# Kernel tuning notes

Measured on AMD Instinct MI355X. Metric: run time of the kernel, lower is better.

Reference implementation:

```python
import jax, jax.numpy as jnp
import numpy as np

# Model/config dims
N_NODE = 500000   # num_node (item vocab)
D      = 100      # opt.hiddenSize
B      = 512      # batch
S      = 50       # session seq len
NS     = 12       # opt.n_sample neighbors per node
HOP    = 1        # opt.n_iter
STEP   = 1        # opt.step (star-graph propagation steps)
LAST   = 3        # opt.last_len
NADJ   = 12       # adjacent items per last item
SCALE  = 1.0 / np.sqrt(D)


def setup_inputs() -> dict:
    key = jax.random.key(0)
    ks = jax.random.split(key, 16)
    stdv = 1.0 / np.sqrt(D)
    u = lambda k, sh: jax.random.uniform(k, sh, jnp.float32, -stdv, stdv)
    return {
        # forward args
        "inputs":     jax.random.randint(ks[0], (B, S), 0, N_NODE),
        "adj":        jax.random.uniform(ks[1], (B, S, S), jnp.float32),
        "item":       jax.random.randint(ks[2], (B, S), 0, N_NODE),
        "last_items": jax.random.randint(ks[3], (B, LAST), 0, N_NODE),
        "adj_items":  jax.random.randint(ks[4], (B, LAST * NADJ), 0, N_NODE),
        # learned params / buffers
        "embedding": u(ks[5], (N_NODE, D)),
        "s":         u(ks[6], (2, 1)),
        "W_star_a":  u(ks[7], (D, D)),
        "W_star_q":  u(ks[8], (D, D)),
        "W_star_k":  u(ks[9], (D, D)),
        "W_g":       u(ks[10], (2 * D, D)),
        "W_l":       u(ks[11], (D, D)),
        "adj_all":   jax.random.randint(ks[12], (N_NODE, NS), 0, N_NODE),
        "num_w":     jax.random.uniform(ks[13], (N_NODE, NS), jnp.float32),
    }


def _l2norm(x):
    # F.normalize(p=2, dim=-1)
    return x / jnp.maximum(jnp.linalg.norm(x, axis=-1, keepdims=True), 1e-12)


def reference(inputs, adj, item, last_items, adj_items,
              embedding, s, W_star_a, W_star_q, W_star_k, W_g, W_l,
              adj_all, num_w):
    # ----- embedding lookup + padding mask -----
    h = embedding[inputs]                                  # [B,S,D]
    mask = (inputs != 0).astype(h.dtype)                   # [B,S]

    # ----- StarAggregator (local branch): star node + gated propagation -----
    denom = jnp.maximum(mask.sum(-1, keepdims=True), 1.0)
    star = (h * mask[..., None]).sum(1) / denom            # [B,D] masked mean
    hl = h
    for _ in range(STEP):
        h_n = jnp.einsum('bst,btd->bsd', adj, hl @ W_star_a)          # neighbor agg
        gate = jax.nn.sigmoid(
            jnp.einsum('bsd,bd->bs', hl @ W_star_q, star @ W_star_k) * SCALE)
        hl = (1.0 - gate)[..., None] * h_n + gate[..., None] * star[:, None, :]
        beta = jnp.einsum('bsd,bd->bs', hl, star) * SCALE
        beta = jax.nn.softmax(jnp.where(mask > 0, beta, -1e9), axis=1)
        star = jnp.einsum('bs,bsd->bd', beta, hl)
    h_local = hl                                           # [B,S,D]

    # ----- GlobalAggregator (hop=1 neighbor-sampling branch) -----
    flat = inputs.reshape(-1)
    neigh_idx = adj_all[flat].reshape(B, S, NS)            # gathered neighbor ids
    neigh_w = num_w[flat].reshape(B, S, NS)                # co-occurrence weights
    neigh = embedding[neigh_idx]                           # [B,S,NS,D]
    alpha = jax.nn.softmax(neigh_w, axis=-1)
    agg = jnp.einsum('bsn,bsnd->bsd', alpha, neigh)        # weighted neighbor sum
    h_global = jax.nn.relu(jnp.concatenate([h, agg], -1) @ W_g)  # [B,S,D]

    # ----- normalize + (eval-mode dropout = identity) + learned 2-way combine -----
    h_local = _l2norm(h_local)
    h_global = _l2norm(h_global)
    output = jnp.einsum('bsdk,ko->bsdo',
                        jnp.stack([h_local, h_global], axis=-1), s)[..., 0]  # [B,S,D]

    # ----- LastAggregator (last-items attention branch) -----
    item_h = embedding[last_items]                         # [B,L,D]
    adj_h = embedding[adj_items].reshape(B, LAST, -1, D)   # [B,L,NADJ,D]
    q = item_h @ W_l
    att = jax.nn.softmax(jnp.einsum('bld,blnd->bln', q, adj_h) * SCALE, axis=-1)
    aggl = jnp.einsum('bln,blnd->bld', att, adj_h)
    last_hidden = (item_h + aggl).mean(axis=1)             # [B,D]

    return output, last_hidden
```

## Files before the change

### kernel.cpp

```cpp
#include <hip/hip_runtime.h>
#include <hip/hip_fp16.h>

#define B_    512
#define S_    50
#define D_    100
#define NS_   12
#define LAST_ 3
#define NADJ_ 12
#define SCALE_ 0.1f

typedef __attribute__((ext_vector_type(4))) float f4;

__device__ __forceinline__ f4 ntload4(const float* p) {
    return __builtin_nontemporal_load((const f4*)p);
}

#define GEMM_STEP(ACC, BUF, K, W0, W1, W2, W3)                                      \
    _Pragma("unroll")                                                                \
    for (int i = 0; i < 5; ++i) {                                                    \
        float4 x = *(const float4*)&BUF[sb + i][K];                                  \
        ACC[i][0] = fmaf(x.x,W0.x, fmaf(x.y,W1.x, fmaf(x.z,W2.x, fmaf(x.w,W3.x, ACC[i][0])))); \
        ACC[i][1] = fmaf(x.x,W0.y, fmaf(x.y,W1.y, fmaf(x.z,W2.y, fmaf(x.w,W3.y, ACC[i][1])))); \
        ACC[i][2] = fmaf(x.x,W0.z, fmaf(x.y,W1.z, fmaf(x.z,W2.z, fmaf(x.w,W3.z, ACC[i][2])))); \
        ACC[i][3] = fmaf(x.x,W0.w, fmaf(x.y,W1.w, fmaf(x.z,W2.w, fmaf(x.w,W3.w, ACC[i][3])))); \
    }

#define AGG_ISSUE(I)                                                                 \
    {   int base = (sb + (I)) * NS_;                                                 \
        _Pragma("unroll")                                                            \
        for (int n = 0; n < NS_; ++n)                                                \
            q[n] = ntload4(emb + nid[base + n] * D_ + d4);                           \
    }
#define AGG_CONSUME(I)                                                               \
    {   int base = (sb + (I)) * NS_;                                                 \
        float mx = -1e30f;                                                           \
        _Pragma("unroll")                                                            \
        for (int n = 0; n < NS_; ++n) mx = fmaxf(mx, alf[base + n]);                 \
        float agw[NS_]; float sm = 0.f;                                              \
        _Pragma("unroll")                                                            \
        for (int n = 0; n < NS_; ++n) { agw[n] = __expf(alf[base + n] - mx); sm += agw[n]; } \
        float inv = 1.f / sm;                                                        \
        _Pragma("unroll")                                                            \
        for (int n = 0; n < NS_; ++n) {                                              \
            float w = agw[n] * inv;                                                  \
            agg[I][0] = fmaf(w, q[n].x, agg[I][0]);                                  \
            agg[I][1] = fmaf(w, q[n].y, agg[I][1]);                                  \
            agg[I][2] = fmaf(w, q[n].z, agg[I][2]);                                  \
            agg[I][3] = fmaf(w, q[n].w, agg[I][3]);                                  \
        }                                                                            \
    }

__global__ __launch_bounds__(256, 3) void fused_all(
    const int* __restrict__ inputs,
    const float* __restrict__ adj,
    const float* __restrict__ emb,
    const int* __restrict__ adj_all,
    const float* __restrict__ num_w,
    const float* __restrict__ sW,
    const float* __restrict__ Wa,
    const float* __restrict__ Wq,
    const float* __restrict__ Wk,
    const float* __restrict__ Wg,
    const int* __restrict__ last_items,
    const int* __restrict__ adj_items,
    const float* __restrict__ Wl,
    float* __restrict__ out)
{
    __shared__ __align__(16) float hL[S_][D_];
    __shared__ __align__(16) float hwa[S_][D_];
    __shared__ __align__(16) union UAS {
        __half adjH[S_][S_];
        float  ssq[S_][25];
    } u;
    __shared__ float star[D_], kb[D_], kq[D_];
    __shared__ float gate[S_], rinv[S_], rinv2[S_];
    __shared__ int   ids[S_];
    __shared__ int   nid[S_ * NS_];
    __shared__ float alf[S_ * NS_];
    __shared__ float denom;

    const int t = threadIdx.x;

    if (blockIdx.x >= B_) {
        const int b = blockIdx.x - B_;
        float* ih  = &hL[0][0];
        float* ah  = &hL[0][0] + 304;
        float* qL  = &hwa[0][0];
        float* att = &u.ssq[0][0];
        int*   li  = ids;
        int*   ai  = nid;

        if (t < LAST_) li[t] = last_items[b * LAST_ + t];
        if (t < LAST_ * NADJ_) ai[t] = adj_items[b * LAST_ * NADJ_ + t];
        __syncthreads();

        for (int e = t; e < LAST_ * 25; e += 256) {
            int l = e / 25, dq = e - l * 25;
            ((f4*)ih)[e] = ntload4(emb + li[l] * D_ + dq * 4);
        }
        for (int e = t; e < LAST_ * NADJ_ * 25; e += 256) {
            int j = e / 25, dq = e - j * 25;
            ((f4*)ah)[e] = ntload4(emb + ai[j] * D_ + dq * 4);
        }
        __syncthreads();

        for (int e = t; e < LAST_ * D_; e += 256) {
            int l = e / D_, d = e - l * D_;
            float a = 0.f;
            for (int k = 0; k < D_; ++k) a = fmaf(ih[l * D_ + k], Wl[k * D_ + d], a);
            qL[e] = a;
        }
        __syncthreads();

        if (t < LAST_ * NADJ_) {
            int l = t / NADJ_;
            const float* ar = ah + t * D_;
            const float* qr = qL + l * D_;
            float a = 0.f;
            for (int d = 0; d < D_; ++d) a = fmaf(qr[d], ar[d], a);
            att[t] = a * SCALE_;
        }
        __syncthreads();

        if (t < LAST_) {
            float mx = -1e30f;
            for (int n = 0; n < NADJ_; ++n) mx = fmaxf(mx, att[t * NADJ_ + n]);
            float ex[NADJ_]; float sm = 0.f;
            for (int n = 0; n < NADJ_; ++n) { ex[n] = __expf(att[t * NADJ_ + n] - mx); sm += ex[n]; }
            float inv = 1.f / sm;
            for (int n = 0; n < NADJ_; ++n) att[t * NADJ_ + n] = ex[n] * inv;
        }
        __syncthreads();

        if (t < D_) {
            float acc = 0.f;
            for (int l = 0; l < LAST_; ++l) {
                float a = ih[l * D_ + t];
                for (int n = 0; n < NADJ_; ++n)
                    a = fmaf(att[l * NADJ_ + n], ah[(l * NADJ_ + n) * D_ + t], a);
                acc += a;
            }
            __builtin_nontemporal_store(acc * (1.f / 3.f),
                                        out + B_ * S_ * D_ + b * D_ + t);
        }
        return;
    }

    const int b = blockIdx.x;
    const float s0 = sW[0], s1 = sW[1];

    const bool act = (t < 250);
    int sg = 0, dg = 0, sb = 0, d4 = 0;
    if (act) { sg = t / 25; dg = t - sg * 25; sb = sg * 5; d4 = dg * 4; }

    const float4* WaQ = (const float4*)Wa;
    float4 wa0, wa1, wa2, wa3;
    if (act) {
        wa0 = WaQ[0 * 25 + dg]; wa1 = WaQ[1 * 25 + dg];
        wa2 = WaQ[2 * 25 + dg]; wa3 = WaQ[3 * 25 + dg];
    }

    if (t < S_) ids[t] = inputs[b * S_ + t];
    __syncthreads();

    if (t < 64) {
        unsigned long long m = __ballot(t < S_ && ids[t] != 0);
        if (t == 0) denom = fmaxf((float)__popcll(m), 1.f);
    }
    for (int e = t; e < S_ * 25; e += 256) {
        int s = e / 25, dq = e - s * 25;
        ((f4*)&hL[0][0])[e] = ntload4(emb + ids[s] * D_ + dq * 4);
    }
    {
        __half2* dst = (__half2*)&u.adjH[0][0];
        const float* src = adj + b * S_ * S_;
        for (int e = t; e < S_ * S_ / 4; e += 256) {
            f4 v = ntload4(src + e * 4);
            dst[2 * e]     = __floats2half2_rn(v.x, v.y);
            dst[2 * e + 1] = __floats2half2_rn(v.z, v.w);
        }
    }
    for (int e = t; e < S_ * NS_; e += 256) {
        int r = e / NS_, n = e - r * NS_;
        nid[e] = adj_all[ids[r] * NS_ + n];
        alf[e] = num_w[ids[r] * NS_ + n];
    }
    __syncthreads();

    f4 q[NS_];
    float agg[5][4] = {};

    if (act) AGG_ISSUE(0)
    if (t < D_) {
        float a = 0.f;
        for (int s = 0; s < S_; ++s) a += (ids[s] != 0) ? hL[s][t] : 0.f;
        star[t] = a / denom;
    }
    __syncthreads();

    if (t < D_) {
        float a = 0.f;
        for (int k = 0; k < D_; ++k) a = fmaf(star[k], Wk[k * D_ + t], a);
        kb[t] = a;
    }
    if (act) { AGG_CONSUME(0) AGG_ISSUE(1) }
    __syncthreads();

    if (t < D_) {
        float a = 0.f;
        const float4* wr = (const float4*)(Wq + t * D_);
#pragma unroll 5
        for (int j = 0; j < 25; ++j) {
            float4 uq = wr[j]; int k = j * 4;
            a = fmaf(uq.x, kb[k + 0], a); a = fmaf(uq.y, kb[k + 1], a);
            a = fmaf(uq.z, kb[k + 2], a); a = fmaf(uq.w, kb[k + 3], a);
        }
        kq[t] = a;
    }
    if (act) { AGG_CONSUME(1) AGG_ISSUE(2) }
    __syncthreads();

    if (t < S_) {
        float a = 0.f;
        const float4* hr = (const float4*)&hL[t][0];
#pragma unroll 5
        for (int j = 0; j < 25; ++j) {
            float4 uq = hr[j]; int k = j * 4;
            a = fmaf(uq.x, kq[k + 0], a); a = fmaf(uq.y, kq[k + 1], a);
            a = fmaf(uq.z, kq[k + 2], a); a = fmaf(uq.w, kq[k + 3], a);
        }
        gate[t] = 1.f / (1.f + __expf(-a * SCALE_));
    }
    if (act) {
        AGG_CONSUME(2)
        float acc[5][4] = {};
        for (int k = 0; k < 96; k += 4) {
            float4 n0 = WaQ[(k + 4) * 25 + dg], n1 = WaQ[(k + 5) * 25 + dg],
                   n2 = WaQ[(k + 6) * 25 + dg], n3 = WaQ[(k + 7) * 25 + dg];
            GEMM_STEP(acc, hL, k, wa0, wa1, wa2, wa3)
            wa0 = n0; wa1 = n1; wa2 = n2; wa3 = n3;
        }
        GEMM_STEP(acc, hL, 96, wa0, wa1, wa2, wa3)
#pragma unroll
        for (int i = 0; i < 5; ++i) {
            float4 v; v.x = acc[i][0]; v.y = acc[i][1]; v.z = acc[i][2]; v.w = acc[i][3];
            *(float4*)&hwa[sb + i][d4] = v;
        }
        AGG_ISSUE(3)
    }
    __syncthreads();

    float hl[5][4] = {};
    if (act) {
        for (int k = 0; k < S_; k += 2) {
            float4 w0 = *(const float4*)&hwa[k][d4];
            float4 w1 = *(const float4*)&hwa[k + 1][d4];
#pragma unroll
            for (int i = 0; i < 5; ++i) {
                float2 a2 = __half22float2(*(const __half2*)&u.adjH[sb + i][k]);
                hl[i][0] = fmaf(a2.x, w0.x, fmaf(a2.y, w1.x, hl[i][0]));
                hl[i][1] = fmaf(a2.x, w0.y, fmaf(a2.y, w1.y, hl[i][1]));
                hl[i][2] = fmaf(a2.x, w0.z, fmaf(a2.y, w1.z, hl[i][2]));
                hl[i][3] = fmaf(a2.x, w0.w, fmaf(a2.y, w1.w, hl[i][3]));
            }
        }
#pragma unroll
        for (int i = 0; i < 5; ++i) {
            float g = gate[sb + i];
#pragma unroll
            for (int j = 0; j < 4; ++j)
                hl[i][j] = (1.f - g) * hl[i][j] + g * star[d4 + j];
        }
        AGG_CONSUME(3) AGG_ISSUE(4)
    }
    __syncthreads();

    const float4* WgQ = (const float4*)Wg;
    float4 wg0, wg1, wg2, wg3;
    if (act) {
        wg0 = WgQ[0 * 25 + dg]; wg1 = WgQ[1 * 25 + dg];
        wg2 = WgQ[2 * 25 + dg]; wg3 = WgQ[3 * 25 + dg];
        AGG_CONSUME(4)
#pragma unroll
        for (int i = 0; i < 5; ++i)
            u.ssq[sb + i][dg] = hl[i][0]*hl[i][0] + hl[i][1]*hl[i][1]
                              + hl[i][2]*hl[i][2] + hl[i][3]*hl[i][3];
#pragma unroll
        for (int i = 0; i < 5; ++i) {
            float4 v; v.x = agg[i][0]; v.y = agg[i][1]; v.z = agg[i][2]; v.w = agg[i][3];
            *(float4*)&hwa[sb + i][d4] = v;
        }
    }
    __syncthreads();

    if (t < S_) {
        float ss = 0.f;
#pragma unroll
        for (int j = 0; j < 25; ++j) ss += u.ssq[t][j];
        rinv[t] = s0 / fmaxf(sqrtf(ss), 1e-12f);
    }
    __syncthreads();

    float o[5][4] = {};
    if (act) {
#pragma unroll
        for (int i = 0; i < 5; ++i) {
            float f = rinv[sb + i];
#pragma unroll
            for (int j = 0; j < 4; ++j) hl[i][j] *= f;
        }
        for (int k = 0; k < 96; k += 4) {
            float4 n0 = WgQ[(k + 4) * 25 + dg], n1 = WgQ[(k + 5) * 25 + dg],
                   n2 = WgQ[(k + 6) * 25 + dg], n3 = WgQ[(k + 7) * 25 + dg];
            GEMM_STEP(o, hL, k, wg0, wg1, wg2, wg3)
            wg0 = n0; wg1 = n1; wg2 = n2; wg3 = n3;
        }
        {
            float4 n0 = WgQ[100 * 25 + dg], n1 = WgQ[101 * 25 + dg],
                   n2 = WgQ[102 * 25 + dg], n3 = WgQ[103 * 25 + dg];
            GEMM_STEP(o, hL, 96, wg0, wg1, wg2, wg3)
            wg0 = n0; wg1 = n1; wg2 = n2; wg3 = n3;
        }
        for (int k = 0; k < 96; k += 4) {
            float4 n0 = WgQ[(100 + k + 4) * 25 + dg], n1 = WgQ[(100 + k + 5) * 25 + dg],
                   n2 = WgQ[(100 + k + 6) * 25 + dg], n3 = WgQ[(100 + k + 7) * 25 + dg];
            GEMM_STEP(o, hwa, k, wg0, wg1, wg2, wg3)
            wg0 = n0; wg1 = n1; wg2 = n2; wg3 = n3;
        }
        GEMM_STEP(o, hwa, 96, wg0, wg1, wg2, wg3)
#pragma unroll
        for (int i = 0; i < 5; ++i) {
#pragma unroll
            for (int j = 0; j < 4; ++j) o[i][j] = fmaxf(o[i][j], 0.f);
            u.ssq[sb + i][dg] = o[i][0]*o[i][0] + o[i][1]*o[i][1]
                              + o[i][2]*o[i][2] + o[i][3]*o[i][3];
        }
    }
    __syncthreads();

    if (t < S_) {
        float ss = 0.f;
#pragma unroll
        for (int j = 0; j < 25; ++j) ss += u.ssq[t][j];
        rinv2[t] = s1 / fmaxf(sqrtf(ss), 1e-12f);
    }
    __syncthreads();

    if (act) {
#pragma unroll
        for (int i = 0; i < 5; ++i) {
            float f = rinv2[sb + i];
            int row = b * S_ + sb + i;
            f4 ov;
            ov.x = hl[i][0] + o[i][0] * f;
            ov.y = hl[i][1] + o[i][1] * f;
            ov.z = hl[i][2] + o[i][2] * f;
            ov.w = hl[i][3] + o[i][3] * f;
            __builtin_nontemporal_store(ov, (f4*)(out + row * D_) + dg);
        }
    }
}

extern "C" void kernel_launch(void* const* d_in, const int* in_sizes, int n_in,
                              void* d_out, int out_size, void* d_ws, size_t ws_size,
                              hipStream_t stream) {
    (void)in_sizes; (void)n_in; (void)out_size; (void)d_ws; (void)ws_size;
    const int* inputs     = (const int*)d_in[0];
    const float* adj      = (const float*)d_in[1];
    const int* last_items = (const int*)d_in[3];
    const int* adj_items  = (const int*)d_in[4];
    const float* emb      = (const float*)d_in[5];
    const float* sW       = (const float*)d_in[6];
    const float* Wa       = (const float*)d_in[7];
    const float* Wq       = (const float*)d_in[8];
    const float* Wk       = (const float*)d_in[9];
    const float* Wg       = (const float*)d_in[10];
    const float* Wl       = (const float*)d_in[11];
    const int* adj_all    = (const int*)d_in[12];
    const float* num_w    = (const float*)d_in[13];

    float* out = (float*)d_out;

    fused_all<<<2 * B_, 256, 0, stream>>>(inputs, adj, emb, adj_all, num_w,
                                          sW, Wa, Wq, Wk, Wg,
                                          last_items, adj_items, Wl, out);
}
```

Before: 343.7 us.

## Reassociate adj·(h·Wa) and precompute Wk·Wq^T product in prep kernel

Reorders the star propagation to compute adj@h first and then multiply by Wa, which lets the adj product start before the gate chain. A small prep kernel fuses Wk and Wq into one 100x100 matrix in workspace, so each block does one matvec instead of two and saves a barrier. The norm-reduction barriers are also merged and rearranged. The cost is an extra kernel launch and a small change in float rounding order.

```diff
diff --git a/kernel.cpp b/kernel.cpp
--- a/kernel.cpp
+++ b/kernel.cpp
@@ -50,6 +50,27 @@
         }                                                                            \
     }
 
+__global__ __launch_bounds__(128) void prep_M(
+    const float* __restrict__ Wq, const float* __restrict__ Wk,
+    float* __restrict__ Mt)
+{
+    __shared__ float wk[D_];
+    const int k = blockIdx.x, t = threadIdx.x;
+    for (int j = t; j < D_; j += 128) wk[j] = Wk[k * D_ + j];
+    __syncthreads();
+    if (t < D_) {
+        const float4* wr = (const float4*)(Wq + t * D_);
+        float a = 0.f;
+#pragma unroll 5
+        for (int j = 0; j < 25; ++j) {
+            float4 u = wr[j]; int jj = j * 4;
+            a = fmaf(u.x, wk[jj + 0], a); a = fmaf(u.y, wk[jj + 1], a);
+            a = fmaf(u.z, wk[jj + 2], a); a = fmaf(u.w, wk[jj + 3], a);
+        }
+        Mt[k * D_ + t] = a;
+    }
+}
+
 __global__ __launch_bounds__(256, 3) void fused_all(
     const int* __restrict__ inputs,
     const float* __restrict__ adj,
@@ -64,6 +85,8 @@
     const int* __restrict__ last_items,
     const int* __restrict__ adj_items,
     const float* __restrict__ Wl,
+    const float* __restrict__ Mt,
+    int useM,
     float* __restrict__ out)
 {
     __shared__ __align__(16) float hL[S_][D_];
@@ -190,7 +213,27 @@
     f4 q[NS_];
     float agg[5][4] = {};
 
-    if (act) AGG_ISSUE(0)
+    if (act) {
+        AGG_ISSUE(0)
+        float acc[5][4] = {};
+        for (int k = 0; k < S_; k += 2) {
+            float4 w0 = *(const float4*)&hL[k][d4];
+            float4 w1 = *(const float4*)&hL[k + 1][d4];
+#pragma unroll
+            for (int i = 0; i < 5; ++i) {
+                float2 a2 = __half22float2(*(const __half2*)&u.adjH[sb + i][k]);
+                acc[i][0] = fmaf(a2.x, w0.x, fmaf(a2.y, w1.x, acc[i][0]));
+                acc[i][1] = fmaf(a2.x, w0.y, fmaf(a2.y, w1.y, acc[i][1]));
+                acc[i][2] = fmaf(a2.x, w0.z, fmaf(a2.y, w1.z, acc[i][2]));
+                acc[i][3] = fmaf(a2.x, w0.w, fmaf(a2.y, w1.w, acc[i][3]));
+            }
+        }
+#pragma unroll
+        for (int i = 0; i < 5; ++i) {
+            float4 v; v.x = acc[i][0]; v.y = acc[i][1]; v.z = acc[i][2]; v.w = acc[i][3];
+            *(float4*)&hwa[sb + i][d4] = v;
+        }
+    }
     if (t < D_) {
         float a = 0.f;
         for (int s = 0; s < S_; ++s) a += (ids[s] != 0) ? hL[s][t] : 0.f;
@@ -198,27 +241,45 @@
     }
     __syncthreads();
 
+    float hn[5][4] = {};
+    if (act) {
+        AGG_CONSUME(0) AGG_ISSUE(1)
+    }
     if (t < D_) {
         float a = 0.f;
-        for (int k = 0; k < D_; ++k) a = fmaf(star[k], Wk[k * D_ + t], a);
-        kb[t] = a;
-    }
-    if (act) { AGG_CONSUME(0) AGG_ISSUE(1) }
-    __syncthreads();
-
-    if (t < D_) {
-        float a = 0.f;
-        const float4* wr = (const float4*)(Wq + t * D_);
+        if (useM) {
+            for (int k = 0; k < D_; ++k) a = fmaf(star[k], Mt[k * D_ + t], a);
+            kq[t] = a;
+        } else {
+            for (int k = 0; k < D_; ++k) a = fmaf(star[k], Wk[k * D_ + t], a);
+            kb[t] = a;
+        }
+    }
+    if (act) {
+        for (int k = 0; k < 96; k += 4) {
+            float4 n0 = WaQ[(k + 4) * 25 + dg], n1 = WaQ[(k + 5) * 25 + dg],
+                   n2 = WaQ[(k + 6) * 25 + dg], n3 = WaQ[(k + 7) * 25 + dg];
+            GEMM_STEP(hn, hwa, k, wa0, wa1, wa2, wa3)
+            wa0 = n0; wa1 = n1; wa2 = n2; wa3 = n3;
+        }
+        GEMM_STEP(hn, hwa, 96, wa0, wa1, wa2, wa3)
+    }
+    __syncthreads();
+
+    if (!useM) {
+        if (t < D_) {
+            float a = 0.f;
+            const float4* wr = (const float4*)(Wq + t * D_);
 #pragma unroll 5
-        for (int j = 0; j < 25; ++j) {
-            float4 uq = wr[j]; int k = j * 4;
-            a = fmaf(uq.x, kb[k + 0], a); a = fmaf(uq.y, kb[k + 1], a);
-            a = fmaf(uq.z, kb[k + 2], a); a = fmaf(uq.w, kb[k + 3], a);
-        }
-        kq[t] = a;
-    }
-    if (act) { AGG_CONSUME(1) AGG_ISSUE(2) }
-    __syncthreads();
+            for (int j = 0; j < 25; ++j) {
+                float4 uq = wr[j]; int k = j * 4;
+                a = fmaf(uq.x, kb[k + 0], a); a = fmaf(uq.y, kb[k + 1], a);
+                a = fmaf(uq.z, kb[k + 2], a); a = fmaf(uq.w, kb[k + 3], a);
+            }
+            kq[t] = a;
+        }
+        __syncthreads();
+    }
 
     if (t < S_) {
         float a = 0.f;
@@ -231,84 +292,57 @@
         }
         gate[t] = 1.f / (1.f + __expf(-a * SCALE_));
     }
-    if (act) {
-        AGG_CONSUME(2)
-        float acc[5][4] = {};
-        for (int k = 0; k < 96; k += 4) {
-            float4 n0 = WaQ[(k + 4) * 25 + dg], n1 = WaQ[(k + 5) * 25 + dg],
-                   n2 = WaQ[(k + 6) * 25 + dg], n3 = WaQ[(k + 7) * 25 + dg];
-            GEMM_STEP(acc, hL, k, wa0, wa1, wa2, wa3)
-            wa0 = n0; wa1 = n1; wa2 = n2; wa3 = n3;
-        }
-        GEMM_STEP(acc, hL, 96, wa0, wa1, wa2, wa3)
-#pragma unroll
-        for (int i = 0; i < 5; ++i) {
-            float4 v; v.x = acc[i][0]; v.y = acc[i][1]; v.z = acc[i][2]; v.w = acc[i][3];
-            *(float4*)&hwa[sb + i][d4] = v;
-        }
-        AGG_ISSUE(3)
-    }
-    __syncthreads();
-
-    float hl[5][4] = {};
-    if (act) {
-        for (int k = 0; k < S_; k += 2) {
-            float4 w0 = *(const float4*)&hwa[k][d4];
-            float4 w1 = *(const float4*)&hwa[k + 1][d4];
-#pragma unroll
-            for (int i = 0; i < 5; ++i) {
-                float2 a2 = __half22float2(*(const __half2*)&u.adjH[sb + i][k]);
-                hl[i][0] = fmaf(a2.x, w0.x, fmaf(a2.y, w1.x, hl[i][0]));
-                hl[i][1] = fmaf(a2.x, w0.y, fmaf(a2.y, w1.y, hl[i][1]));
-                hl[i][2] = fmaf(a2.x, w0.z, fmaf(a2.y, w1.z, hl[i][2]));
-                hl[i][3] = fmaf(a2.x, w0.w, fmaf(a2.y, w1.w, hl[i][3]));
-            }
-        }
+    if (act) { AGG_CONSUME(1) AGG_ISSUE(2) }
+    __syncthreads();
+
+    float hl[5][4];
+    if (act) {
 #pragma unroll
         for (int i = 0; i < 5; ++i) {
             float g = gate[sb + i];
 #pragma unroll
             for (int j = 0; j < 4; ++j)
-                hl[i][j] = (1.f - g) * hl[i][j] + g * star[d4 + j];
-        }
-        AGG_CONSUME(3) AGG_ISSUE(4)
+                hl[i][j] = (1.f - g) * hn[i][j] + g * star[d4 + j];
+            u.ssq[sb + i][dg] = hl[i][0]*hl[i][0] + hl[i][1]*hl[i][1]
+                              + hl[i][2]*hl[i][2] + hl[i][3]*hl[i][3];
+        }
+        AGG_CONSUME(2) AGG_ISSUE(3)
     }
     __syncthreads();
 
     const float4* WgQ = (const float4*)Wg;
     float4 wg0, wg1, wg2, wg3;
+    if (t < S_) {
+        float ss = 0.f;
+#pragma unroll
+        for (int j = 0; j < 25; ++j) ss += u.ssq[t][j];
+        rinv[t] = s0 / fmaxf(sqrtf(ss), 1e-12f);
+    }
     if (act) {
         wg0 = WgQ[0 * 25 + dg]; wg1 = WgQ[1 * 25 + dg];
         wg2 = WgQ[2 * 25 + dg]; wg3 = WgQ[3 * 25 + dg];
+        AGG_CONSUME(3) AGG_ISSUE(4)
+    }
+    __syncthreads();
+
+    if (act) {
         AGG_CONSUME(4)
-#pragma unroll
-        for (int i = 0; i < 5; ++i)
-            u.ssq[sb + i][dg] = hl[i][0]*hl[i][0] + hl[i][1]*hl[i][1]
-                              + hl[i][2]*hl[i][2] + hl[i][3]*hl[i][3];
 #pragma unroll
         for (int i = 0; i < 5; ++i) {
             float4 v; v.x = agg[i][0]; v.y = agg[i][1]; v.z = agg[i][2]; v.w = agg[i][3];
             *(float4*)&hwa[sb + i][d4] = v;
         }
-    }
-    __syncthreads();
-
-    if (t < S_) {
-        float ss = 0.f;
-#pragma unroll
-        for (int j = 0; j < 25; ++j) ss += u.ssq[t][j];
-        rinv[t] = s0 / fmaxf(sqrtf(ss), 1e-12f);
+#pragma unroll
+        for (int i = 0; i < 5; ++i) {
+            float f = rinv[sb + i];
+#pragma unroll
+            for (int j = 0; j < 4; ++j) hl[i][j] *= f;
+        }
     }
     __syncthreads();
 
     float o[5][4] = {};
     if (act) {
-#pragma unroll
-        for (int i = 0; i < 5; ++i) {
-            float f = rinv[sb + i];
-#pragma unroll
-            for (int j = 0; j < 4; ++j) hl[i][j] *= f;
-        }
         for (int k = 0; k < 96; k += 4) {
             float4 n0 = WgQ[(k + 4) * 25 + dg], n1 = WgQ[(k + 5) * 25 + dg],
                    n2 = WgQ[(k + 6) * 25 + dg], n3 = WgQ[(k + 7) * 25 + dg];
@@ -364,7 +398,7 @@
 extern "C" void kernel_launch(void* const* d_in, const int* in_sizes, int n_in,
                               void* d_out, int out_size, void* d_ws, size_t ws_size,
                               hipStream_t stream) {
-    (void)in_sizes; (void)n_in; (void)out_size; (void)d_ws; (void)ws_size;
+    (void)in_sizes; (void)n_in; (void)out_size;
     const int* inputs     = (const int*)d_in[0];
     const float* adj      = (const float*)d_in[1];
     const int* last_items = (const int*)d_in[3];
@@ -381,7 +415,12 @@
 
     float* out = (float*)d_out;
 
+    const int useM = (d_ws != nullptr && ws_size >= (size_t)(D_ * D_ * 4)) ? 1 : 0;
+    float* Mt = (float*)d_ws;
+    if (useM) prep_M<<<D_, 128, 0, stream>>>(Wq, Wk, Mt);
+
     fused_all<<<2 * B_, 256, 0, stream>>>(inputs, adj, emb, adj_all, num_w,
                                           sW, Wa, Wq, Wk, Wg,
-                                          last_items, adj_items, Wl, out);
+                                          last_items, adj_items, Wl,
+                                          Mt, useM, out);
 }
```

Result: no change. 344.0 us (+0.1%).

## Reorder adj·(h·Wa) to (adj·h)·Wa, store h and weights in half, raise occupancy

Applied to the files above, without the earlier changes.

Computes the neighbour aggregation as (adj·h)·Wa instead of adj·(h·Wa). This moves the adjacency product ahead of the weight GEMM so it overlaps the first gather. The embedding tile and the co-occurrence weights are kept in shared memory as fp16, and several shared buffers are unioned to cut LDS usage. Launch bounds rise from 3 to 4 blocks per CU. The fp16 storage of h lowers precision, and the simpler unpipelined weight loads may expose more global-load latency.

```diff
diff --git a/kernel.cpp b/kernel.cpp
--- a/kernel.cpp
+++ b/kernel.cpp
@@ -13,6 +13,13 @@
 
 __device__ __forceinline__ f4 ntload4(const float* p) {
     return __builtin_nontemporal_load((const f4*)p);
+}
+
+__device__ __forceinline__ float4 ldh4(const __half* p) {
+    float2 fa = __half22float2(*(const __half2*)p);
+    float2 fb = __half22float2(*(const __half2*)(p + 2));
+    float4 r; r.x = fa.x; r.y = fa.y; r.z = fb.x; r.w = fb.y;
+    return r;
 }
 
 #define GEMM_STEP(ACC, BUF, K, W0, W1, W2, W3)                                      \
@@ -24,6 +31,15 @@
         ACC[i][2] = fmaf(x.x,W0.z, fmaf(x.y,W1.z, fmaf(x.z,W2.z, fmaf(x.w,W3.z, ACC[i][2])))); \
         ACC[i][3] = fmaf(x.x,W0.w, fmaf(x.y,W1.w, fmaf(x.z,W2.w, fmaf(x.w,W3.w, ACC[i][3])))); \
     }
+#define GEMM_STEP_H(ACC, BUF, K, W0, W1, W2, W3)                                    \
+    _Pragma("unroll")                                                                \
+    for (int i = 0; i < 5; ++i) {                                                    \
+        float4 x = ldh4(&BUF[sb + i][K]);                                            \
+        ACC[i][0] = fmaf(x.x,W0.x, fmaf(x.y,W1.x, fmaf(x.z,W2.x, fmaf(x.w,W3.x, ACC[i][0])))); \
+        ACC[i][1] = fmaf(x.x,W0.y, fmaf(x.y,W1.y, fmaf(x.z,W2.y, fmaf(x.w,W3.y, ACC[i][1])))); \
+        ACC[i][2] = fmaf(x.x,W0.z, fmaf(x.y,W1.z, fmaf(x.z,W2.z, fmaf(x.w,W3.z, ACC[i][2])))); \
+        ACC[i][3] = fmaf(x.x,W0.w, fmaf(x.y,W1.w, fmaf(x.z,W2.w, fmaf(x.w,W3.w, ACC[i][3])))); \
+    }
 
 #define AGG_ISSUE(I)                                                                 \
     {   int base = (sb + (I)) * NS_;                                                 \
@@ -33,16 +49,17 @@
     }
 #define AGG_CONSUME(I)                                                               \
     {   int base = (sb + (I)) * NS_;                                                 \
-        float mx = -1e30f;                                                           \
+        float av[NS_]; float mx = -1e30f;                                            \
         _Pragma("unroll")                                                            \
-        for (int n = 0; n < NS_; ++n) mx = fmaxf(mx, alf[base + n]);                 \
-        float agw[NS_]; float sm = 0.f;                                              \
+        for (int n = 0; n < NS_; ++n) { av[n] = __half2float(alfH[base + n]);        \
+                                        mx = fmaxf(mx, av[n]); }                     \
+        float sm = 0.f;                                                              \
         _Pragma("unroll")                                                            \
-        for (int n = 0; n < NS_; ++n) { agw[n] = __expf(alf[base + n] - mx); sm += agw[n]; } \
+        for (int n = 0; n < NS_; ++n) { av[n] = __expf(av[n] - mx); sm += av[n]; }   \
         float inv = 1.f / sm;                                                        \
         _Pragma("unroll")                                                            \
         for (int n = 0; n < NS_; ++n) {                                              \
-            float w = agw[n] * inv;                                                  \
+            float w = av[n] * inv;                                                   \
             agg[I][0] = fmaf(w, q[n].x, agg[I][0]);                                  \
             agg[I][1] = fmaf(w, q[n].y, agg[I][1]);                                  \
             agg[I][2] = fmaf(w, q[n].z, agg[I][2]);                                  \
@@ -50,7 +67,7 @@
         }                                                                            \
     }
 
-__global__ __launch_bounds__(256, 3) void fused_all(
+__global__ __launch_bounds__(256, 4) void fused_all(
     const int* __restrict__ inputs,
     const float* __restrict__ adj,
     const float* __restrict__ emb,
@@ -66,78 +83,78 @@
     const float* __restrict__ Wl,
     float* __restrict__ out)
 {
-    __shared__ __align__(16) float hL[S_][D_];
-    __shared__ __align__(16) float hwa[S_][D_];
-    __shared__ __align__(16) union UAS {
+    __shared__ __align__(16) union HU {
+        __half h[S_][D_];
+        float  ihf[LAST_][D_];
+    } hu;
+    __shared__ __align__(16) union WU {
+        float w[S_][D_];
+        float ah[LAST_][NADJ_][D_];
+    } wu;
+    __shared__ __align__(16) union US {
         __half adjH[S_][S_];
         float  ssq[S_][25];
+        float  att[LAST_][NADJ_];
     } u;
-    __shared__ float star[D_], kb[D_], kq[D_];
+    __shared__ __align__(16) float sk[300];
     __shared__ float gate[S_], rinv[S_], rinv2[S_];
     __shared__ int   ids[S_];
     __shared__ int   nid[S_ * NS_];
-    __shared__ float alf[S_ * NS_];
+    __shared__ __half alfH[S_ * NS_];
     __shared__ float denom;
 
     const int t = threadIdx.x;
 
     if (blockIdx.x >= B_) {
         const int b = blockIdx.x - B_;
-        float* ih  = &hL[0][0];
-        float* ah  = &hL[0][0] + 304;
-        float* qL  = &hwa[0][0];
-        float* att = &u.ssq[0][0];
-        int*   li  = ids;
-        int*   ai  = nid;
-
-        if (t < LAST_) li[t] = last_items[b * LAST_ + t];
-        if (t < LAST_ * NADJ_) ai[t] = adj_items[b * LAST_ * NADJ_ + t];
+        if (t < LAST_) ids[t] = last_items[b * LAST_ + t];
+        if (t < LAST_ * NADJ_) nid[t] = adj_items[b * LAST_ * NADJ_ + t];
         __syncthreads();
 
         for (int e = t; e < LAST_ * 25; e += 256) {
             int l = e / 25, dq = e - l * 25;
-            ((f4*)ih)[e] = ntload4(emb + li[l] * D_ + dq * 4);
+            *((f4*)&hu.ihf[0][0] + e) = ntload4(emb + ids[l] * D_ + dq * 4);
         }
         for (int e = t; e < LAST_ * NADJ_ * 25; e += 256) {
             int j = e / 25, dq = e - j * 25;
-            ((f4*)ah)[e] = ntload4(emb + ai[j] * D_ + dq * 4);
+            *((f4*)&wu.ah[0][0][0] + e) = ntload4(emb + nid[j] * D_ + dq * 4);
         }
         __syncthreads();
 
         for (int e = t; e < LAST_ * D_; e += 256) {
             int l = e / D_, d = e - l * D_;
             float a = 0.f;
-            for (int k = 0; k < D_; ++k) a = fmaf(ih[l * D_ + k], Wl[k * D_ + d], a);
-            qL[e] = a;
+            for (int k = 0; k < D_; ++k) a = fmaf(hu.ihf[l][k], Wl[k * D_ + d], a);
+            sk[e] = a;
         }
         __syncthreads();
 
         if (t < LAST_ * NADJ_) {
-            int l = t / NADJ_;
-            const float* ar = ah + t * D_;
-            const float* qr = qL + l * D_;
+            int l = t / NADJ_, n = t - l * NADJ_;
+            const float* ar = &wu.ah[l][n][0];
+            const float* qr = &sk[l * D_];
             float a = 0.f;
             for (int d = 0; d < D_; ++d) a = fmaf(qr[d], ar[d], a);
-            att[t] = a * SCALE_;
+            u.att[l][n] = a * SCALE_;
         }
         __syncthreads();
 
         if (t < LAST_) {
             float mx = -1e30f;
-            for (int n = 0; n < NADJ_; ++n) mx = fmaxf(mx, att[t * NADJ_ + n]);
+            for (int n = 0; n < NADJ_; ++n) mx = fmaxf(mx, u.att[t][n]);
             float ex[NADJ_]; float sm = 0.f;
-            for (int n = 0; n < NADJ_; ++n) { ex[n] = __expf(att[t * NADJ_ + n] - mx); sm += ex[n]; }
+            for (int n = 0; n < NADJ_; ++n) { ex[n] = __expf(u.att[t][n] - mx); sm += ex[n]; }
             float inv = 1.f / sm;
-            for (int n = 0; n < NADJ_; ++n) att[t * NADJ_ + n] = ex[n] * inv;
+            for (int n = 0; n < NADJ_; ++n) u.att[t][n] = ex[n] * inv;
         }
         __syncthreads();
 
         if (t < D_) {
             float acc = 0.f;
             for (int l = 0; l < LAST_; ++l) {
-                float a = ih[l * D_ + t];
+                float a = hu.ihf[l][t];
                 for (int n = 0; n < NADJ_; ++n)
-                    a = fmaf(att[l * NADJ_ + n], ah[(l * NADJ_ + n) * D_ + t], a);
+                    a = fmaf(u.att[l][n], wu.ah[l][n][t], a);
                 acc += a;
             }
             __builtin_nontemporal_store(acc * (1.f / 3.f),
@@ -148,18 +165,14 @@
 
     const int b = blockIdx.x;
     const float s0 = sW[0], s1 = sW[1];
+    float* star = sk;
+    float* kb   = sk + 100;
+    float* kq   = sk + 200;
 
     const bool act = (t < 250);
     int sg = 0, dg = 0, sb = 0, d4 = 0;
     if (act) { sg = t / 25; dg = t - sg * 25; sb = sg * 5; d4 = dg * 4; }
 
-    const float4* WaQ = (const float4*)Wa;
-    float4 wa0, wa1, wa2, wa3;
-    if (act) {
-        wa0 = WaQ[0 * 25 + dg]; wa1 = WaQ[1 * 25 + dg];
-        wa2 = WaQ[2 * 25 + dg]; wa3 = WaQ[3 * 25 + dg];
-    }
-
     if (t < S_) ids[t] = inputs[b * S_ + t];
     __syncthreads();
 
@@ -169,7 +182,10 @@
     }
     for (int e = t; e < S_ * 25; e += 256) {
         int s = e / 25, dq = e - s * 25;
-        ((f4*)&hL[0][0])[e] = ntload4(emb + ids[s] * D_ + dq * 4);
+        f4 v = ntload4(emb + ids[s] * D_ + dq * 4);
+        __half2* dst = (__half2*)&hu.h[s][dq * 4];
+        dst[0] = __floats2half2_rn(v.x, v.y);
+        dst[1] = __floats2half2_rn(v.z, v.w);
     }
     {
         __half2* dst = (__half2*)&u.adjH[0][0];
@@ -182,28 +198,57 @@
     }
     for (int e = t; e < S_ * NS_; e += 256) {
         int r = e / NS_, n = e - r * NS_;
-        nid[e] = adj_all[ids[r] * NS_ + n];
-        alf[e] = num_w[ids[r] * NS_ + n];
+        nid[e]  = adj_all[ids[r] * NS_ + n];
+        alfH[e] = __float2half(num_w[ids[r] * NS_ + n]);
     }
     __syncthreads();
 
     f4 q[NS_];
     float agg[5][4] = {};
 
-    if (act) AGG_ISSUE(0)
+    if (act) {
+        AGG_ISSUE(0)
+        float acc[5][4] = {};
+        for (int k = 0; k < S_; k += 2) {
+            float4 w0 = ldh4(&hu.h[k][d4]);
+            float4 w1 = ldh4(&hu.h[k + 1][d4]);
+#pragma unroll
+            for (int i = 0; i < 5; ++i) {
+                float2 a2 = __half22float2(*(const __half2*)&u.adjH[sb + i][k]);
+                acc[i][0] = fmaf(a2.x, w0.x, fmaf(a2.y, w1.x, acc[i][0]));
+                acc[i][1] = fmaf(a2.x, w0.y, fmaf(a2.y, w1.y, acc[i][1]));
+                acc[i][2] = fmaf(a2.x, w0.z, fmaf(a2.y, w1.z, acc[i][2]));
+                acc[i][3] = fmaf(a2.x, w0.w, fmaf(a2.y, w1.w, acc[i][3]));
+            }
+        }
+#pragma unroll
+        for (int i = 0; i < 5; ++i) {
+            float4 v; v.x = acc[i][0]; v.y = acc[i][1]; v.z = acc[i][2]; v.w = acc[i][3];
+            *(float4*)&wu.w[sb + i][d4] = v;
+        }
+    }
     if (t < D_) {
         float a = 0.f;
-        for (int s = 0; s < S_; ++s) a += (ids[s] != 0) ? hL[s][t] : 0.f;
+        for (int s = 0; s < S_; ++s) a += (ids[s] != 0) ? __half2float(hu.h[s][t]) : 0.f;
         star[t] = a / denom;
     }
     __syncthreads();
 
+    float hn[5][4] = {};
+    if (act) { AGG_CONSUME(0) AGG_ISSUE(1) }
     if (t < D_) {
         float a = 0.f;
         for (int k = 0; k < D_; ++k) a = fmaf(star[k], Wk[k * D_ + t], a);
         kb[t] = a;
     }
-    if (act) { AGG_CONSUME(0) AGG_ISSUE(1) }
+    if (act) {
+        const float4* WaQ = (const float4*)Wa;
+        for (int k = 0; k < D_; k += 4) {
+            float4 w0 = WaQ[(k + 0) * 25 + dg], w1 = WaQ[(k + 1) * 25 + dg],
+                   w2 = WaQ[(k + 2) * 25 + dg], w3 = WaQ[(k + 3) * 25 + dg];
+            GEMM_STEP(hn, wu.w, k, w0, w1, w2, w3)
+        }
+    }
     __syncthreads();
 
     if (t < D_) {
@@ -222,74 +267,28 @@
 
     if (t < S_) {
         float a = 0.f;
-        const float4* hr = (const float4*)&hL[t][0];
-#pragma unroll 5
-        for (int j = 0; j < 25; ++j) {
-            float4 uq = hr[j]; int k = j * 4;
-            a = fmaf(uq.x, kq[k + 0], a); a = fmaf(uq.y, kq[k + 1], a);
-            a = fmaf(uq.z, kq[k + 2], a); a = fmaf(uq.w, kq[k + 3], a);
+#pragma unroll 10
+        for (int j = 0; j < 50; ++j) {
+            float2 hv = __half22float2(*(const __half2*)&hu.h[t][2 * j]);
+            a = fmaf(hv.x, kq[2 * j], fmaf(hv.y, kq[2 * j + 1], a));
         }
         gate[t] = 1.f / (1.f + __expf(-a * SCALE_));
     }
-    if (act) {
-        AGG_CONSUME(2)
-        float acc[5][4] = {};
-        for (int k = 0; k < 96; k += 4) {
-            float4 n0 = WaQ[(k + 4) * 25 + dg], n1 = WaQ[(k + 5) * 25 + dg],
-                   n2 = WaQ[(k + 6) * 25 + dg], n3 = WaQ[(k + 7) * 25 + dg];
-            GEMM_STEP(acc, hL, k, wa0, wa1, wa2, wa3)
-            wa0 = n0; wa1 = n1; wa2 = n2; wa3 = n3;
-        }
-        GEMM_STEP(acc, hL, 96, wa0, wa1, wa2, wa3)
-#pragma unroll
-        for (int i = 0; i < 5; ++i) {
-            float4 v; v.x = acc[i][0]; v.y = acc[i][1]; v.z = acc[i][2]; v.w = acc[i][3];
-            *(float4*)&hwa[sb + i][d4] = v;
-        }
-        AGG_ISSUE(3)
-    }
-    __syncthreads();
-
-    float hl[5][4] = {};
-    if (act) {
-        for (int k = 0; k < S_; k += 2) {
-            float4 w0 = *(const float4*)&hwa[k][d4];
-            float4 w1 = *(const float4*)&hwa[k + 1][d4];
-#pragma unroll
-            for (int i = 0; i < 5; ++i) {
-                float2 a2 = __half22float2(*(const __half2*)&u.adjH[sb + i][k]);
-                hl[i][0] = fmaf(a2.x, w0.x, fmaf(a2.y, w1.x, hl[i][0]));
-                hl[i][1] = fmaf(a2.x, w0.y, fmaf(a2.y, w1.y, hl[i][1]));
-                hl[i][2] = fmaf(a2.x, w0.z, fmaf(a2.y, w1.z, hl[i][2]));
-                hl[i][3] = fmaf(a2.x, w0.w, fmaf(a2.y, w1.w, hl[i][3]));
-            }
-        }
+    if (act) { AGG_CONSUME(2) AGG_ISSUE(3) }
+    __syncthreads();
+
+    float hl[5][4];
+    if (act) {
 #pragma unroll
         for (int i = 0; i < 5; ++i) {
             float g = gate[sb + i];
 #pragma unroll
             for (int j = 0; j < 4; ++j)
-                hl[i][j] = (1.f - g) * hl[i][j] + g * star[d4 + j];
-        }
-        AGG_CONSUME(3) AGG_ISSUE(4)
-    }
-    __syncthreads();
-
-    const float4* WgQ = (const float4*)Wg;
-    float4 wg0, wg1, wg2, wg3;
-    if (act) {
-        wg0 = WgQ[0 * 25 + dg]; wg1 = WgQ[1 * 25 + dg];
-        wg2 = WgQ[2 * 25 + dg]; wg3 = WgQ[3 * 25 + dg];
-        AGG_CONSUME(4)
-#pragma unroll
-        for (int i = 0; i < 5; ++i)
+                hl[i][j] = (1.f - g) * hn[i][j] + g * star[d4 + j];
             u.ssq[sb + i][dg] = hl[i][0]*hl[i][0] + hl[i][1]*hl[i][1]
                               + hl[i][2]*hl[i][2] + hl[i][3]*hl[i][3];
-#pragma unroll
-        for (int i = 0; i < 5; ++i) {
-            float4 v; v.x = agg[i][0]; v.y = agg[i][1]; v.z = agg[i][2]; v.w = agg[i][3];
-            *(float4*)&hwa[sb + i][d4] = v;
-        }
+        }
+        AGG_CONSUME(3) AGG_ISSUE(4)
     }
     __syncthreads();
 
@@ -299,35 +298,37 @@
         for (int j = 0; j < 25; ++j) ss += u.ssq[t][j];
         rinv[t] = s0 / fmaxf(sqrtf(ss), 1e-12f);
     }
+    if (act) { AGG_CONSUME(4) }
+    __syncthreads();
+
+    if (act) {
+#pragma unroll
+        for (int i = 0; i < 5; ++i) {
+            float4 v; v.x = agg[i][0]; v.y = agg[i][1]; v.z = agg[i][2]; v.w = agg[i][3];
+            *(float4*)&wu.w[sb + i][d4] = v;
+        }
+#pragma unroll
+        for (int i = 0; i < 5; ++i) {
+            float f = rinv[sb + i];
+#pragma unroll
+            for (int j = 0; j < 4; ++j) hl[i][j] *= f;
+        }
+    }
     __syncthreads();
 
     float o[5][4] = {};
     if (act) {
-#pragma unroll
-        for (int i = 0; i < 5; ++i) {
-            float f = rinv[sb + i];
-#pragma unroll
-            for (int j = 0; j < 4; ++j) hl[i][j] *= f;
-        }
-        for (int k = 0; k < 96; k += 4) {
-            float4 n0 = WgQ[(k + 4) * 25 + dg], n1 = WgQ[(k + 5) * 25 + dg],
-                   n2 = WgQ[(k + 6) * 25 + dg], n3 = WgQ[(k + 7) * 25 + dg];
-            GEMM_STEP(o, hL, k, wg0, wg1, wg2, wg3)
-            wg0 = n0; wg1 = n1; wg2 = n2; wg3 = n3;
-        }
-        {
-            float4 n0 = WgQ[100 * 25 + dg], n1 = WgQ[101 * 25 + dg],
-                   n2 = WgQ[102 * 25 + dg], n3 = WgQ[103 * 25 + dg];
-            GEMM_STEP(o, hL, 96, wg0, wg1, wg2, wg3)
-            wg0 = n0; wg1 = n1; wg2 = n2; wg3 = n3;
-        }
-        for (int k = 0; k < 96; k += 4) {
-            float4 n0 = WgQ[(100 + k + 4) * 25 + dg], n1 = WgQ[(100 + k + 5) * 25 + dg],
-                   n2 = WgQ[(100 + k + 6) * 25 + dg], n3 = WgQ[(100 + k + 7) * 25 + dg];
-            GEMM_STEP(o, hwa, k, wg0, wg1, wg2, wg3)
-            wg0 = n0; wg1 = n1; wg2 = n2; wg3 = n3;
-        }
-        GEMM_STEP(o, hwa, 96, wg0, wg1, wg2, wg3)
+        const float4* WgQ = (const float4*)Wg;
+        for (int k = 0; k < D_; k += 4) {
+            float4 w0 = WgQ[(k + 0) * 25 + dg], w1 = WgQ[(k + 1) * 25 + dg],
+                   w2 = WgQ[(k + 2) * 25 + dg], w3 = WgQ[(k + 3) * 25 + dg];
+            GEMM_STEP_H(o, hu.h, k, w0, w1, w2, w3)
+        }
+        for (int k = 0; k < D_; k += 4) {
+            float4 w0 = WgQ[(D_ + k + 0) * 25 + dg], w1 = WgQ[(D_ + k + 1) * 25 + dg],
+                   w2 = WgQ[(D_ + k + 2) * 25 + dg], w3 = WgQ[(D_ + k + 3) * 25 + dg];
+            GEMM_STEP(o, wu.w, k, w0, w1, w2, w3)
+        }
 #pragma unroll
         for (int i = 0; i < 5; ++i) {
 #pragma unroll
```

Result: slower. 383.9 us (+11.7%).
